# Kernel tuning notes

Measured on AMD Instinct MI355X. Metric: run time of the kernel, lower is better.

The kernel has to match this reference:

```python
import jax, jax.numpy as jnp
import numpy as np

D_MODEL = 256
N_HEADS = 8
B, S = 8, 2048
TEMP = jnp.sqrt(jnp.float32(D_MODEL))  # ScaledDotProductAttention(temperature=d_model) -> sqrt(d_model)
NEG = jnp.float32(-1e9)


def setup_inputs() -> dict:
    key = jax.random.key(0)
    ks = jax.random.split(key, 12)
    dh = D_MODEL * N_HEADS
    sc_in = 1.0 / np.sqrt(D_MODEL)
    sc_out = 1.0 / np.sqrt(dh)
    return {
        "query": jax.random.normal(ks[0], (B, S, D_MODEL), jnp.float32),
        "key": jax.random.normal(ks[1], (B, S, D_MODEL), jnp.float32),
        "value": jax.random.normal(ks[2], (B, S, D_MODEL), jnp.float32),
        "mask": jax.random.bernoulli(ks[3], 0.9, (B, S)),
        "Wq": jax.random.normal(ks[4], (D_MODEL, dh), jnp.float32) * sc_in,
        "bq": jnp.zeros((dh,), jnp.float32),
        "Wk": jax.random.normal(ks[5], (D_MODEL, dh), jnp.float32) * sc_in,
        "bk": jnp.zeros((dh,), jnp.float32),
        "Wv": jax.random.normal(ks[6], (D_MODEL, dh), jnp.float32) * sc_in,
        "bv": jnp.zeros((dh,), jnp.float32),
        "Wo": jax.random.normal(ks[7], (dh, D_MODEL), jnp.float32) * sc_out,
        "bo": jnp.zeros((D_MODEL,), jnp.float32),
    }


def reference(query, key, value, mask, Wq, bq, Wk, bk, Wv, bv, Wo, bo):
    nb = query.shape[0]
    # projections: (B,S,d) @ (d, d*H) -> view (B,S,H,d)
    q = (query @ Wq + bq).reshape(nb, -1, N_HEADS, D_MODEL)
    k = (key @ Wk + bk).reshape(nb, -1, N_HEADS, D_MODEL)
    v = (value @ Wv + bv).reshape(nb, -1, N_HEADS, D_MODEL)
    # torch.matmul on (B,S,H,d): batched over (B,S) -> per-position HxH attention
    attn = jnp.einsum('bshd,bsgd->bshg', q, k) / TEMP
    m = mask[:, :, None, None]  # (B,S,1,1) broadcast, as in mask.view(B,-1,1,1)
    attn = jnp.where(m, attn, NEG)
    attn = jax.nn.softmax(attn, axis=-1)  # dropout p=0 -> identity
    x = jnp.einsum('bshg,bsgd->bshd', attn, v)  # (B,S,H,d)
    # x.transpose(1,2).contiguous().view(B,-1,d*H)
    x = jnp.transpose(x, (0, 2, 1, 3)).reshape(nb, -1, D_MODEL * N_HEADS)
    return x @ Wo + bo
```

## Files before the change

kernel.cpp:

```cpp
#include <hip/hip_runtime.h>
#include <hip/hip_bf16.h>

typedef __hip_bfloat16 bf16;
typedef short bf16x8 __attribute__((ext_vector_type(8)));
typedef float f32x4 __attribute__((ext_vector_type(4)));

#define MFMA16(a,b,c) __builtin_amdgcn_mfma_f32_16x16x32_bf16(a,b,c,0,0,0)

__device__ __forceinline__ unsigned short f2us(float x){
    union{__hip_bfloat16 h; unsigned short u;} c; c.h = __float2bfloat16(x); return c.u;
}
__device__ __forceinline__ float us2f(unsigned short u){
    union{unsigned short u; __hip_bfloat16 h;} c; c.u = u; return __bfloat162float(c.h);
}
__device__ __forceinline__ uint4 pack8(float4 a, float4 b){
    union{unsigned short us[8]; uint4 v;} p;
    p.us[0]=f2us(a.x); p.us[1]=f2us(a.y); p.us[2]=f2us(a.z); p.us[3]=f2us(a.w);
    p.us[4]=f2us(b.x); p.us[5]=f2us(b.y); p.us[6]=f2us(b.z); p.us[7]=f2us(b.w);
    return p.v;
}

__global__ __launch_bounds__(256) void prep_kernel(
    const float* __restrict__ Wq, const float* __restrict__ Wk,
    const float* __restrict__ Wv, const float* __restrict__ bq,
    const float* __restrict__ bk, const float* __restrict__ bv,
    const float* __restrict__ Wo,
    bf16* __restrict__ WqT, bf16* __restrict__ WkT, bf16* __restrict__ WvT,
    float* __restrict__ bqp, float* __restrict__ bkp, float* __restrict__ bvp,
    bf16* __restrict__ WoT)
{
    __shared__ float T[64][68];
    const int tid = threadIdx.x, bx = blockIdx.x;
    if (bx < 384) {
        const int mat = bx / 128, rem = bx % 128;
        const int c0 = (rem >> 5) * 64, n0 = (rem & 31) * 64;
        const float* W = (mat == 0) ? Wq : (mat == 1) ? Wk : Wv;
        bf16* WT = (mat == 0) ? WqT : (mat == 1) ? WkT : WvT;
        #pragma unroll
        for (int it = 0; it < 4; ++it) {
            int pp = tid + (it << 8);
            int cl = pp >> 4, n4 = (pp & 15) * 4;
            float4 f = *(const float4*)(W + (size_t)(c0 + cl) * 2048 + n0 + n4);
            T[cl][n4] = f.x; T[cl][n4+1] = f.y; T[cl][n4+2] = f.z; T[cl][n4+3] = f.w;
        }
        __syncthreads();
        const int h = n0 >> 8, d0 = n0 & 255;
        #pragma unroll
        for (int it = 0; it < 2; ++it) {
            int pp = tid + (it << 8);
            int j = pp >> 3, g = pp & 7;
            union{unsigned short us[8]; uint4 v;} pk;
            #pragma unroll
            for (int u = 0; u < 8; ++u) pk.us[u] = f2us(T[g*8+u][j]);
            *(uint4*)(WT + (size_t)((d0 + j) * 8 + h) * 256 + c0 + g * 8) = pk.v;
        }
    } else if (bx < 387) {
        const int mat = bx - 384;
        const float* src = (mat == 0) ? bq : (mat == 1) ? bk : bv;
        float* dst = (mat == 0) ? bqp : (mat == 1) ? bkp : bvp;
        for (int n = tid; n < 2048; n += 256)
            dst[(n & 255) * 8 + (n >> 8)] = src[n];
    } else {
        const int idx = bx - 387;
        const int k0 = (idx >> 2) * 64, c0 = (idx & 3) * 64;
        #pragma unroll
        for (int it = 0; it < 4; ++it) {
            int pp = tid + (it << 8);
            int kl = pp >> 4, c4 = (pp & 15) * 4;
            float4 f = *(const float4*)(Wo + (size_t)(k0 + kl) * 256 + c0 + c4);
            T[kl][c4] = f.x; T[kl][c4+1] = f.y; T[kl][c4+2] = f.z; T[kl][c4+3] = f.w;
        }
        __syncthreads();
        #pragma unroll
        for (int it = 0; it < 2; ++it) {
            int pp = tid + (it << 8);
            int j = pp >> 3, g = pp & 7;
            union{unsigned short us[8]; uint4 v;} pk;
            #pragma unroll
            for (int u = 0; u < 8; ++u) pk.us[u] = f2us(T[g*8+u][j]);
            *(uint4*)(WoT + (size_t)(c0 + j) * 2048 + k0 + g * 8) = pk.v;
        }
    }
}

__global__ __launch_bounds__(512, 2) void qk_kernel(
    const float* __restrict__ Qin, const float* __restrict__ Kin,
    const int* __restrict__ mask,
    const bf16* __restrict__ WqT, const bf16* __restrict__ WkT,
    const float* __restrict__ bqp, const float* __restrict__ bkp,
    float* __restrict__ w)
{
    __shared__ __align__(16) char smem[147456];
    char* const Xq = smem;
    char* const Xk = smem + 32768;
    char* const QT = smem + 65536;
    char* const KT = smem + 106496;
    float* const RED = (float*)smem;

    const int tid  = threadIdx.x;
    const int wid  = tid >> 6, lane = tid & 63;
    const int quad = lane >> 4, l15 = lane & 15;
    const int tok0 = blockIdx.x * 64;

    #pragma unroll
    for (int it = 0; it < 4; ++it) {
        int pp = tid + (it << 9);
        int row = pp >> 5, g = pp & 31;
        const float* s = Qin + (size_t)(tok0 + row) * 256 + g * 8;
        *(uint4*)(Xq + row * 512 + ((g ^ (row & 7)) << 4)) =
            pack8(*(const float4*)s, *(const float4*)(s + 4));
        s = Kin + (size_t)(tok0 + row) * 256 + g * 8;
        *(uint4*)(Xk + row * 512 + ((g ^ (row & 7)) << 4)) =
            pack8(*(const float4*)s, *(const float4*)(s + 4));
    }
    __syncthreads();

    f32x4 sacc[4];
    #pragma unroll
    for (int p = 0; p < 4; ++p)
        #pragma unroll
        for (int i = 0; i < 4; ++i) sacc[p][i] = 0.f;

    for (int Cp = 0; Cp < 8; ++Cp) {
        f32x4 accq[4][2], acck[4][2];
        #pragma unroll
        for (int mt = 0; mt < 4; ++mt)
            #pragma unroll
            for (int nt = 0; nt < 2; ++nt)
                #pragma unroll
                for (int i = 0; i < 4; ++i) { accq[mt][nt][i] = 0.f; acck[mt][nt][i] = 0.f; }
        #pragma unroll
        for (int Ks = 0; Ks < 8; ++Ks) {
            bf16x8 bq[2], bk[2];
            #pragma unroll
            for (int nt = 0; nt < 2; ++nt) {
                const size_t boff =
                    (size_t)(Cp * 256 + wid * 32 + nt * 16 + l15) * 256 + Ks * 32 + quad * 8;
                bq[nt] = *(const bf16x8*)(WqT + boff);
                bk[nt] = *(const bf16x8*)(WkT + boff);
            }
            #pragma unroll
            for (int mt = 0; mt < 4; ++mt) {
                int row = mt * 16 + l15;
                int G = (Ks * 4 + quad) ^ (row & 7);
                bf16x8 aq = *(const bf16x8*)(Xq + row * 512 + (G << 4));
                bf16x8 ak = *(const bf16x8*)(Xk + row * 512 + (G << 4));
                #pragma unroll
                for (int nt = 0; nt < 2; ++nt) {
                    accq[mt][nt] = MFMA16(aq, bq[nt], accq[mt][nt]);
                    acck[mt][nt] = MFMA16(ak, bk[nt], acck[mt][nt]);
                }
            }
        }
        #pragma unroll
        for (int nt = 0; nt < 2; ++nt) {
            const int p2 = wid * 32 + nt * 16 + l15;
            const int rowoff = p2 * 160 + ((p2 >> 6) & 3) * 8;
            const float biq = bqp[Cp * 256 + p2];
            const float bik = bkp[Cp * 256 + p2];
            #pragma unroll
            for (int mt = 0; mt < 4; ++mt) {
                int t0 = mt * 16 + quad * 4;
                union{unsigned short us[4]; uint2 v;} pq, pk;
                #pragma unroll
                for (int i = 0; i < 4; ++i) {
                    pq.us[i] = f2us(accq[mt][nt][i] + biq);
                    pk.us[i] = f2us(acck[mt][nt][i] + bik);
                }
                *(uint2*)(QT + rowoff + t0 * 2) = pq.v;
                *(uint2*)(KT + rowoff + t0 * 2) = pk.v;
            }
        }
        __syncthreads();
        #pragma unroll
        for (int pp2 = 0; pp2 < 4; ++pp2) {
            int tq = 2 * (wid * 4 + pp2) + (l15 >> 3);
            union{unsigned short us[8]; bf16x8 v;} Aq, Bk;
            #pragma unroll
            for (int j = 0; j < 8; ++j) {
                int p2 = (quad * 8 + j) * 8 + (l15 & 7);
                int off = p2 * 160 + ((p2 >> 6) & 3) * 8 + tq * 2;
                Aq.us[j] = *(const unsigned short*)(QT + off);
                Bk.us[j] = *(const unsigned short*)(KT + off);
            }
            sacc[pp2] = MFMA16(Aq.v, Bk.v, sacc[pp2]);
        }
        __syncthreads();
    }

    if ((quad >> 1) == (l15 >> 3)) {
        #pragma unroll
        for (int pp2 = 0; pp2 < 4; ++pp2) {
            int tl = (wid * 4 + pp2) * 2 + (l15 >> 3);
            #pragma unroll
            for (int i = 0; i < 4; ++i)
                RED[tl * 68 + ((quad & 1) * 4 + i) * 8 + (l15 & 7)] = sacc[pp2][i];
        }
    }
    __syncthreads();
    {
        const int tl = tid >> 3, hh = tid & 7;
        const int mk = mask[tok0 + tl];
        const float* r = RED + tl * 68 + hh * 8;
        float m = r[0];
        #pragma unroll
        for (int g = 1; g < 8; ++g) m = fmaxf(m, r[g]);
        float e[8], sum = 0.f;
        #pragma unroll
        for (int g = 0; g < 8; ++g) { e[g] = __expf((r[g] - m) * 0.0625f); sum += e[g]; }
        float inv = 1.f / sum;
        float o[8];
        #pragma unroll
        for (int g = 0; g < 8; ++g) o[g] = mk ? e[g] * inv : 0.125f;
        float* wp = w + (size_t)(tok0 + tl) * 64 + hh * 8;
        *(float4*)wp = make_float4(o[0], o[1], o[2], o[3]);
        *(float4*)(wp + 4) = make_float4(o[4], o[5], o[6], o[7]);
    }
}

__global__ __launch_bounds__(512) void v_attn_kernel(
    const float* __restrict__ Vin,
    const bf16* __restrict__ WvT, const float* __restrict__ bvp,
    const float* __restrict__ w, bf16* __restrict__ A)
{
    __shared__ __align__(16) char smem[66560];
    char* const Xv = smem;
    char* const VT = smem + 32768;
    char* const xS = smem + 50176;

    const int tid  = threadIdx.x;
    const int wid  = tid >> 6, lane = tid & 63;
    const int quad = lane >> 4, l15 = lane & 15;
    const int tok0 = blockIdx.x * 64;
    const int t6   = tid & 63, dg = tid >> 6;

    #pragma unroll
    for (int it = 0; it < 4; ++it) {
        int pp = tid + (it << 9);
        int row = pp >> 5, g = pp & 31;
        const float* s = Vin + (size_t)(tok0 + row) * 256 + g * 8;
        *(uint4*)(Xv + row * 512 + ((g ^ (row & 7)) << 4)) =
            pack8(*(const float4*)s, *(const float4*)(s + 4));
    }
    float wv[64];
    {
        const float* wp = w + (size_t)(tok0 + t6) * 64;
        #pragma unroll
        for (int i = 0; i < 16; ++i) {
            float4 f = ((const float4*)wp)[i];
            wv[i*4] = f.x; wv[i*4+1] = f.y; wv[i*4+2] = f.z; wv[i*4+3] = f.w;
        }
    }
    __syncthreads();

    const int pll = wid * 16 + l15;

    for (int C = 0; C < 16; ++C) {
        f32x4 acc[4];
        #pragma unroll
        for (int mt = 0; mt < 4; ++mt)
            #pragma unroll
            for (int i = 0; i < 4; ++i) acc[mt][i] = 0.f;
        #pragma unroll
        for (int Ks = 0; Ks < 8; ++Ks) {
            bf16x8 b = *(const bf16x8*)(WvT + (size_t)(C * 128 + pll) * 256 + Ks * 32 + quad * 8);
            #pragma unroll
            for (int mt = 0; mt < 4; ++mt) {
                int row = mt * 16 + l15;
                int G = (Ks * 4 + quad) ^ (row & 7);
                bf16x8 a = *(const bf16x8*)(Xv + row * 512 + (G << 4));
                acc[mt] = MFMA16(a, b, acc[mt]);
            }
        }
        const float biv = bvp[C * 128 + pll];
        #pragma unroll
        for (int mt = 0; mt < 4; ++mt) {
            int t0 = mt * 16 + quad * 4;
            union{unsigned short us[4]; uint2 v;} pk;
            #pragma unroll
            for (int i = 0; i < 4; ++i) pk.us[i] = f2us(acc[mt][i] + biv);
            *(uint2*)(VT + pll * 136 + t0 * 2) = pk.v;
        }
        __syncthreads();
        #pragma unroll
        for (int dd = 0; dd < 2; ++dd) {
            int d = dg * 2 + dd;
            float vv[8];
            #pragma unroll
            for (int g = 0; g < 8; ++g)
                vv[g] = us2f(*(const unsigned short*)(VT + (d * 8 + g) * 136 + t6 * 2));
            #pragma unroll
            for (int h = 0; h < 8; ++h) {
                float x = 0.f;
                #pragma unroll
                for (int g = 0; g < 8; ++g) x = fmaf(wv[h * 8 + g], vv[g], x);
                int u = (h * 2 + (d >> 3)) ^ (t6 & 15);
                *(unsigned short*)(xS + t6 * 256 + u * 16 + (d & 7) * 2) = f2us(x);
            }
        }
        __syncthreads();
        {
            int t = tid >> 3, hh = tid & 7;
            int tok = tok0 + t;
            int b = tok >> 11, sr = tok & 2047, sg = sr >> 3, j = sr & 7;
            size_t r = ((size_t)b << 11) + hh * 256 + sg;
            bf16* dst = A + r * 2048 + j * 256 + C * 16;
            int u0 = (hh * 2) ^ (t & 15), u1 = (hh * 2 + 1) ^ (t & 15);
            *(uint4*)dst       = *(const uint4*)(xS + t * 256 + u0 * 16);
            *(uint4*)(dst + 8) = *(const uint4*)(xS + t * 256 + u1 * 16);
        }
    }
}

__global__ __launch_bounds__(256) void outproj_kernel(
    const bf16* __restrict__ A, const bf16* __restrict__ WoT,
    const float* __restrict__ Wo, const float* __restrict__ bo,
    float* __restrict__ Out)
{
    __shared__ __align__(16) char smem[24576];
    char* const AsS = smem;
    char* const Ws  = smem + 8192;

    const int tid = threadIdx.x;
    const int wave = tid >> 6, lane = tid & 63, quad = lane >> 4, l15 = lane & 15;
    const int R = blockIdx.x >> 1, C = blockIdx.x & 1;
    const int row0 = R * 64, col0 = C * 128;

    f32x4 acc[4][2];
    #pragma unroll
    for (int mt = 0; mt < 4; ++mt)
        #pragma unroll
        for (int nt = 0; nt < 2; ++nt)
            #pragma unroll
            for (int i = 0; i < 4; ++i) acc[mt][nt][i] = 0.f;

    for (int kc = 0; kc < 32; ++kc) {
        __syncthreads();
        #pragma unroll
        for (int it = 0; it < 2; ++it) {
            int pp = tid + (it << 8);
            int rho = pp >> 3, g = pp & 7;
            *(uint4*)(AsS + rho * 128 + ((g ^ (rho & 7)) << 4)) =
                *(const uint4*)(A + (size_t)(row0 + rho) * 2048 + kc * 64 + g * 8);
        }
        if (WoT != nullptr) {
            #pragma unroll
            for (int it = 0; it < 4; ++it) {
                int pp = tid + (it << 8);
                int cl = pp >> 3, g = pp & 7;
                *(uint4*)(Ws + cl * 128 + ((g ^ (cl & 7)) << 4)) =
                    *(const uint4*)(WoT + (size_t)(col0 + cl) * 2048 + kc * 64 + g * 8);
            }
        } else {
            #pragma unroll
            for (int it = 0; it < 8; ++it) {
                int pp = tid + (it << 8);
                int kl = pp >> 5, c4 = (pp & 31) * 4;
                float4 f = *(const float4*)(Wo + (size_t)(kc * 64 + kl) * 256 + col0 + c4);
                float fv[4] = {f.x, f.y, f.z, f.w};
                #pragma unroll
                for (int u = 0; u < 4; ++u) {
                    int cl = c4 + u;
                    *(unsigned short*)(Ws + cl * 128 + (((kl >> 3) ^ (cl & 7)) << 4) + (kl & 7) * 2)
                        = f2us(fv[u]);
                }
            }
        }
        __syncthreads();
        #pragma unroll
        for (int ks = 0; ks < 2; ++ks) {
            bf16x8 a[4], b[2];
            #pragma unroll
            for (int mt = 0; mt < 4; ++mt) {
                int row = mt * 16 + l15;
                int G = (ks * 4 + quad) ^ (row & 7);
                a[mt] = *(const bf16x8*)(AsS + row * 128 + (G << 4));
            }
            #pragma unroll
            for (int nt = 0; nt < 2; ++nt) {
                int cl = wave * 32 + nt * 16 + l15;
                int G = (ks * 4 + quad) ^ (cl & 7);
                b[nt] = *(const bf16x8*)(Ws + cl * 128 + (G << 4));
            }
            #pragma unroll
            for (int mt = 0; mt < 4; ++mt)
                #pragma unroll
                for (int nt = 0; nt < 2; ++nt)
                    acc[mt][nt] = MFMA16(a[mt], b[nt], acc[mt][nt]);
        }
    }
    #pragma unroll
    for (int nt = 0; nt < 2; ++nt) {
        int col = col0 + wave * 32 + nt * 16 + l15;
        float bias = bo[col];
        #pragma unroll
        for (int mt = 0; mt < 4; ++mt) {
            int r0 = row0 + mt * 16 + quad * 4;
            #pragma unroll
            for (int i = 0; i < 4; ++i)
                Out[(size_t)(r0 + i) * 256 + col] = acc[mt][nt][i] + bias;
        }
    }
}

extern "C" void kernel_launch(void* const* d_in, const int* in_sizes, int n_in,
                              void* d_out, int out_size, void* d_ws, size_t ws_size,
                              hipStream_t stream) {
    const float* query = (const float*)d_in[0];
    const float* key   = (const float*)d_in[1];
    const float* value = (const float*)d_in[2];
    const int*   mask  = (const int*)  d_in[3];
    const float* Wq = (const float*)d_in[4];  const float* bq = (const float*)d_in[5];
    const float* Wk = (const float*)d_in[6];  const float* bk = (const float*)d_in[7];
    const float* Wv = (const float*)d_in[8];  const float* bv = (const float*)d_in[9];
    const float* Wo = (const float*)d_in[10]; const float* bo = (const float*)d_in[11];

    char* dc = (char*)d_out;
    bf16*  WqT = (bf16*)dc;
    bf16*  WkT = (bf16*)(dc + 1048576);
    bf16*  WvT = (bf16*)(dc + 2097152);
    float* bqp = (float*)(dc + 3145728);
    float* bkp = (float*)(dc + 3153920);
    float* bvp = (float*)(dc + 3162112);
    float* w   = (float*)(dc + 3170304);

    bf16* A = (bf16*)d_ws;
    const bool big = ws_size >= (67108864ull + 1048576ull);
    bf16* WoT = big ? (bf16*)((char*)d_ws + 67108864) : nullptr;

    prep_kernel<<<big ? 515 : 387, 256, 0, stream>>>(
        Wq, Wk, Wv, bq, bk, bv, Wo, WqT, WkT, WvT, bqp, bkp, bvp, WoT);
    qk_kernel<<<256, 512, 0, stream>>>(
        query, key, mask, WqT, WkT, bqp, bkp, w);
    v_attn_kernel<<<256, 512, 0, stream>>>(value, WvT, bvp, w, A);
    outproj_kernel<<<512, 256, 0, stream>>>(A, WoT, Wo, bo, (float*)d_out);
}
```

Before: 304.3 us.

## Fuse output projection into attention-value kernel, removing intermediate A buffer

```diff
diff --git a/kernel.cpp b/kernel.cpp
--- a/kernel.cpp
+++ b/kernel.cpp
@@ -218,10 +218,11 @@
     }
 }
 
-__global__ __launch_bounds__(512) void v_attn_kernel(
+__global__ __launch_bounds__(512, 2) void av_kernel(
     const float* __restrict__ Vin,
     const bf16* __restrict__ WvT, const float* __restrict__ bvp,
-    const float* __restrict__ w, bf16* __restrict__ A)
+    const float* __restrict__ w, const bf16* __restrict__ WoT,
+    const float* __restrict__ bo, float* __restrict__ Out)
 {
     __shared__ __align__(16) char smem[66560];
     char* const Xv = smem;
@@ -255,6 +256,14 @@
 
     const int pll = wid * 16 + l15;
 
+    f32x4 oacc[4][2];
+    #pragma unroll
+    for (int mt = 0; mt < 4; ++mt)
+        #pragma unroll
+        for (int nt = 0; nt < 2; ++nt)
+            #pragma unroll
+            for (int i = 0; i < 4; ++i) oacc[mt][nt][i] = 0.f;
+
     for (int C = 0; C < 16; ++C) {
         f32x4 acc[4];
         #pragma unroll
@@ -299,106 +308,43 @@
             }
         }
         __syncthreads();
-        {
-            int t = tid >> 3, hh = tid & 7;
-            int tok = tok0 + t;
-            int b = tok >> 11, sr = tok & 2047, sg = sr >> 3, j = sr & 7;
-            size_t r = ((size_t)b << 11) + hh * 256 + sg;
-            bf16* dst = A + r * 2048 + j * 256 + C * 16;
-            int u0 = (hh * 2) ^ (t & 15), u1 = (hh * 2 + 1) ^ (t & 15);
-            *(uint4*)dst       = *(const uint4*)(xS + t * 256 + u0 * 16);
-            *(uint4*)(dst + 8) = *(const uint4*)(xS + t * 256 + u1 * 16);
-        }
-    }
-}
-
-__global__ __launch_bounds__(256) void outproj_kernel(
-    const bf16* __restrict__ A, const bf16* __restrict__ WoT,
-    const float* __restrict__ Wo, const float* __restrict__ bo,
-    float* __restrict__ Out)
-{
-    __shared__ __align__(16) char smem[24576];
-    char* const AsS = smem;
-    char* const Ws  = smem + 8192;
-
-    const int tid = threadIdx.x;
-    const int wave = tid >> 6, lane = tid & 63, quad = lane >> 4, l15 = lane & 15;
-    const int R = blockIdx.x >> 1, C = blockIdx.x & 1;
-    const int row0 = R * 64, col0 = C * 128;
-
-    f32x4 acc[4][2];
-    #pragma unroll
-    for (int mt = 0; mt < 4; ++mt)
-        #pragma unroll
-        for (int nt = 0; nt < 2; ++nt)
-            #pragma unroll
-            for (int i = 0; i < 4; ++i) acc[mt][nt][i] = 0.f;
-
-    for (int kc = 0; kc < 32; ++kc) {
-        __syncthreads();
-        #pragma unroll
-        for (int it = 0; it < 2; ++it) {
-            int pp = tid + (it << 8);
-            int rho = pp >> 3, g = pp & 7;
-            *(uint4*)(AsS + rho * 128 + ((g ^ (rho & 7)) << 4)) =
-                *(const uint4*)(A + (size_t)(row0 + rho) * 2048 + kc * 64 + g * 8);
-        }
-        if (WoT != nullptr) {
-            #pragma unroll
-            for (int it = 0; it < 4; ++it) {
-                int pp = tid + (it << 8);
-                int cl = pp >> 3, g = pp & 7;
-                *(uint4*)(Ws + cl * 128 + ((g ^ (cl & 7)) << 4)) =
-                    *(const uint4*)(WoT + (size_t)(col0 + cl) * 2048 + kc * 64 + g * 8);
-            }
-        } else {
-            #pragma unroll
-            for (int it = 0; it < 8; ++it) {
-                int pp = tid + (it << 8);
-                int kl = pp >> 5, c4 = (pp & 31) * 4;
-                float4 f = *(const float4*)(Wo + (size_t)(kc * 64 + kl) * 256 + col0 + c4);
-                float fv[4] = {f.x, f.y, f.z, f.w};
-                #pragma unroll
-                for (int u = 0; u < 4; ++u) {
-                    int cl = c4 + u;
-                    *(unsigned short*)(Ws + cl * 128 + (((kl >> 3) ^ (cl & 7)) << 4) + (kl & 7) * 2)
-                        = f2us(fv[u]);
-                }
-            }
-        }
-        __syncthreads();
-        #pragma unroll
-        for (int ks = 0; ks < 2; ++ks) {
-            bf16x8 a[4], b[2];
+        #pragma unroll
+        for (int m = 0; m < 4; ++m) {
+            const int j  = 2 * m + (quad >> 1);
+            const int k0 = j * 256 + C * 16 + (quad & 1) * 8;
+            bf16x8 bfr[2];
+            #pragma unroll
+            for (int nt = 0; nt < 2; ++nt) {
+                int c = wid * 32 + nt * 16 + l15;
+                bfr[nt] = *(const bf16x8*)(WoT + (size_t)c * 2048 + k0);
+            }
             #pragma unroll
             for (int mt = 0; mt < 4; ++mt) {
-                int row = mt * 16 + l15;
-                int G = (ks * 4 + quad) ^ (row & 7);
-                a[mt] = *(const bf16x8*)(AsS + row * 128 + (G << 4));
-            }
-            #pragma unroll
-            for (int nt = 0; nt < 2; ++nt) {
-                int cl = wave * 32 + nt * 16 + l15;
-                int G = (ks * 4 + quad) ^ (cl & 7);
-                b[nt] = *(const bf16x8*)(Ws + cl * 128 + (G << 4));
-            }
-            #pragma unroll
-            for (int mt = 0; mt < 4; ++mt)
+                int h = mt * 2 + (l15 >> 3);
+                int t = (l15 & 7) * 8 + j;
+                int u = (h * 2 + (quad & 1)) ^ (t & 15);
+                bf16x8 afr = *(const bf16x8*)(xS + t * 256 + u * 16);
                 #pragma unroll
                 for (int nt = 0; nt < 2; ++nt)
-                    acc[mt][nt] = MFMA16(a[mt], b[nt], acc[mt][nt]);
-        }
-    }
+                    oacc[mt][nt] = MFMA16(afr, bfr[nt], oacc[mt][nt]);
+            }
+        }
+    }
+
+    const int b = tok0 >> 11, sg0 = (tok0 & 2047) >> 3;
     #pragma unroll
     for (int nt = 0; nt < 2; ++nt) {
-        int col = col0 + wave * 32 + nt * 16 + l15;
-        float bias = bo[col];
+        int c = wid * 32 + nt * 16 + l15;
+        float bias = bo[c];
         #pragma unroll
         for (int mt = 0; mt < 4; ++mt) {
-            int r0 = row0 + mt * 16 + quad * 4;
-            #pragma unroll
-            for (int i = 0; i < 4; ++i)
-                Out[(size_t)(r0 + i) * 256 + col] = acc[mt][nt][i] + bias;
+            #pragma unroll
+            for (int i = 0; i < 4; ++i) {
+                int rr = mt * 16 + quad * 4 + i;
+                int h = rr >> 3, sgl = rr & 7;
+                size_t r = ((size_t)b << 11) + h * 256 + sg0 + sgl;
+                Out[r * 256 + c] = oacc[mt][nt][i] + bias;
+            }
         }
     }
 }
@@ -415,23 +361,20 @@
     const float* Wv = (const float*)d_in[8];  const float* bv = (const float*)d_in[9];
     const float* Wo = (const float*)d_in[10]; const float* bo = (const float*)d_in[11];
 
-    char* dc = (char*)d_out;
-    bf16*  WqT = (bf16*)dc;
-    bf16*  WkT = (bf16*)(dc + 1048576);
-    bf16*  WvT = (bf16*)(dc + 2097152);
-    float* bqp = (float*)(dc + 3145728);
-    float* bkp = (float*)(dc + 3153920);
-    float* bvp = (float*)(dc + 3162112);
-    float* w   = (float*)(dc + 3170304);
-
-    bf16* A = (bf16*)d_ws;
-    const bool big = ws_size >= (67108864ull + 1048576ull);
-    bf16* WoT = big ? (bf16*)((char*)d_ws + 67108864) : nullptr;
-
-    prep_kernel<<<big ? 515 : 387, 256, 0, stream>>>(
+    char* ws = (char*)d_ws;
+    bf16*  WoT = (bf16*)ws;
+    bf16*  WqT = (bf16*)(ws + 1048576);
+    bf16*  WkT = (bf16*)(ws + 2097152);
+    bf16*  WvT = (bf16*)(ws + 3145728);
+    float* bqp = (float*)(ws + 4194304);
+    float* bkp = (float*)(ws + 4202496);
+    float* bvp = (float*)(ws + 4210688);
+    float* w   = (float*)(ws + 4218880);
+
+    prep_kernel<<<515, 256, 0, stream>>>(
         Wq, Wk, Wv, bq, bk, bv, Wo, WqT, WkT, WvT, bqp, bkp, bvp, WoT);
     qk_kernel<<<256, 512, 0, stream>>>(
         query, key, mask, WqT, WkT, bqp, bkp, w);
-    v_attn_kernel<<<256, 512, 0, stream>>>(value, WvT, bvp, w, A);
-    outproj_kernel<<<512, 256, 0, stream>>>(A, WoT, Wo, bo, (float*)d_out);
-}
+    av_kernel<<<256, 512, 0, stream>>>(
+        value, WvT, bvp, w, WoT, bo, (float*)d_out);
+}
```

Result: faster. 273.0 us (-10.3%).
